# Kernel tuning notes

Hardware: AMD Instinct MI355X
Metric: run time of the kernel (lower is better)

The kernel has to match this reference:

```python
import jax, jax.numpy as jnp
import numpy as np

N = 3000          # num_sample (nodes)
N_OMICS = 3000    # input feature dims for both omics
ENC1, ENC2, NZ = 256, 128, 64


def _xavier(key, fan_in, fan_out):
    limit = float(np.sqrt(6.0 / (fan_in + fan_out)))
    return jax.random.uniform(key, (fan_in, fan_out), jnp.float32, -limit, limit)


def setup_inputs() -> dict:
    key = jax.random.key(0)
    ks = jax.random.split(key, 20)
    inp = {
        "omics_1": jax.random.normal(ks[0], (N, N_OMICS), jnp.float32),
        "omics_2": jax.random.normal(ks[1], (N, N_OMICS), jnp.float32),
    }
    # random dense adjacency, row-normalized (as a typical normalized graph operator)
    for i, name in enumerate(["adj_feature_omics1", "adj_feature_omics2",
                              "adj_spatial_omics1", "adj_spatial_omics2"]):
        a = jax.random.uniform(ks[2 + i], (N, N), jnp.float32)
        inp[name] = a / jnp.sum(a, axis=1, keepdims=True)
    # GNNLayer weights for the four GAE encoders (xavier uniform, as in reset_parameters)
    dims = [(N_OMICS, ENC1), (ENC1, ENC2), (ENC2, NZ)]
    kidx = 6
    for enc in ["f1", "f2", "s1", "s2"]:
        for li, (fi, fo) in enumerate(dims, start=1):
            inp[f"w_{enc}_{li}"] = _xavier(ks[kidx], fi, fo)
            kidx += 1
    return inp


def _gae_encoder(x, adj, w1, w2, w3):
    # GNNLayer: support = act(x @ W); out = spmm(adj, support). Dropout is identity (eval).
    z = adj @ jnp.tanh(x @ w1)          # [N, ENC1]
    z = adj @ jnp.tanh(z @ w2)          # [N, ENC2]
    z = adj @ (z @ w3)                  # [N, NZ]  (no activation on layer 3)
    adj_hat = jax.nn.sigmoid(z @ z.T)   # [N, N]
    return z, adj_hat


def reference(omics_1, omics_2,
              adj_feature_omics1, adj_feature_omics2,
              adj_spatial_omics1, adj_spatial_omics2,
              w_f1_1, w_f1_2, w_f1_3,
              w_f2_1, w_f2_2, w_f2_3,
              w_s1_1, w_s1_2, w_s1_3,
              w_s2_1, w_s2_2, w_s2_3):
    _, a1 = _gae_encoder(omics_1, adj_feature_omics1, w_f1_1, w_f1_2, w_f1_3)
    _, a2 = _gae_encoder(omics_2, adj_feature_omics2, w_f2_1, w_f2_2, w_f2_3)
    _, a3 = _gae_encoder(omics_1, adj_spatial_omics1, w_s1_1, w_s1_2, w_s1_3)
    _, a4 = _gae_encoder(omics_2, adj_spatial_omics2, w_s2_1, w_s2_2, w_s2_3)
    # stacked reconstructed adjacencies from the four encoders [4, N, N]
    return jnp.stack([a1, a2, a3, a4], axis=0)
```

## Files before the change

kernel.cpp:

```cpp
#include <hip/hip_runtime.h>
#include <stdint.h>
#include <stddef.h>


typedef __attribute__((ext_vector_type(8))) _Float16 half8;
typedef __attribute__((ext_vector_type(4))) float f32x4;

#define PAD 3072
#define MR  3000
#define ADJ_STRIDE ((size_t)PAD * PAD)

static __device__ __forceinline__ void async_cp16(const _Float16* g, _Float16* l) {
    __builtin_amdgcn_global_load_lds((const __attribute__((address_space(1))) void*)g,
                                     (__attribute__((address_space(3))) void*)l, 16, 0, 0);
}

struct PrepArgs {
    const float* X[2]; _Float16* Xh;
    const float* Wsrc[12];
    _Float16* Wdst[3];
};

__global__ __launch_bounds__(256) void prep(PrepArgs p) {
    __shared__ _Float16 lt[64 * 64];
    const int b = blockIdx.x;
    const int t = threadIdx.x;
    if (b < 4608) {
        const int which = b / 2304;
        const int idx = (b - which * 2304) * 256 + t;
        const int row = idx / 192;
        const int c0  = (idx - row * 192) * 16;
        const float* sp = p.X[which] + (size_t)row * MR + c0;
        _Float16* d = p.Xh + (size_t)which * ADJ_STRIDE + (size_t)row * PAD + c0;
        half8 h0, h1;
        const bool rok = row < MR;
        if (rok && c0 < MR) {
            f32x4 v0 = __builtin_nontemporal_load((const f32x4*)sp);
            f32x4 v1 = __builtin_nontemporal_load((const f32x4*)(sp + 4));
            #pragma unroll
            for (int j = 0; j < 4; ++j) { h0[j] = (_Float16)v0[j]; h0[4 + j] = (_Float16)v1[j]; }
        } else {
            #pragma unroll
            for (int j = 0; j < 8; ++j) h0[j] = (_Float16)0.f;
        }
        if (rok && c0 + 8 < MR) {
            f32x4 v2 = __builtin_nontemporal_load((const f32x4*)(sp + 8));
            f32x4 v3 = __builtin_nontemporal_load((const f32x4*)(sp + 12));
            #pragma unroll
            for (int j = 0; j < 4; ++j) { h1[j] = (_Float16)v2[j]; h1[4 + j] = (_Float16)v3[j]; }
        } else {
            #pragma unroll
            for (int j = 0; j < 8; ++j) h1[j] = (_Float16)0.f;
        }
        *(half8*)d = h0;
        *(half8*)(d + 8) = h1;
    } else {
        const int b2  = b - 4608;
        const int enc = b2 / 204;
        int rem = b2 - enc * 204;
        const float* src; _Float16* dst; int fi, fo, ldk, kt, rt;
        if (rem < 192) {
            src = p.Wsrc[enc * 3 + 0]; dst = p.Wdst[0] + (size_t)enc * 256 * PAD;
            fi = MR; fo = 256; ldk = PAD; kt = rem >> 2; rt = rem & 3;
        } else if (rem < 200) {
            rem -= 192;
            src = p.Wsrc[enc * 3 + 1]; dst = p.Wdst[1] + (size_t)enc * 128 * 256;
            fi = 256; fo = 128; ldk = 256; kt = rem >> 1; rt = rem & 1;
        } else {
            rem -= 200;
            src = p.Wsrc[enc * 3 + 2]; dst = p.Wdst[2] + (size_t)enc * 128 * 128;
            fi = 128; fo = 64; ldk = 128; kt = rem >> 1; rt = rem & 1;
        }
        const int k0 = kt * 64, r0 = rt * 64;
        {
            const int kr = t >> 2, cc = (t & 3) << 4;
            const int gk = k0 + kr;
            const bool kok = gk < fi;
            #pragma unroll
            for (int j = 0; j < 16; ++j) {
                const int gr = r0 + cc + j;
                const float v = (kok && gr < fo) ? src[(size_t)gk * fo + gr] : 0.f;
                lt[(cc + j) * 64 + kr] = (_Float16)v;
            }
        }
        __syncthreads();
        {
            const int rr = t >> 2, kk = (t & 3) << 4;
            half8 a  = *(half8*)&lt[rr * 64 + kk];
            half8 bb = *(half8*)&lt[rr * 64 + kk + 8];
            _Float16* dp = dst + (size_t)(r0 + rr) * ldk + k0 + kk;
            *(half8*)dp = a;
            *(half8*)(dp + 8) = bb;
        }
    }
}

struct GArgs {
    const _Float16* Aall; size_t aStride; int aMask;
    const _Float16* Ball; size_t bStride; int bMask;
    void* Call; size_t cStride;
    int M, Ncols, Kp, lda, ldb, ldc, mBound, nBound;
};

template<int ACT, int OMODE, int S>
static __device__ __forceinline__
void gemm_body(const GArgs& ga, int bx, int by, int bz, _Float16* smem)
{
    _Float16* As = smem;
    _Float16* Bs = smem + 8192;

    const int z   = bz;
    const int e   = z / S;
    const int ksl = z - e * S;
    const int Kslice = ga.Kp / S;
    const int kbase  = ksl * Kslice;

    const _Float16* A = ga.Aall + (size_t)(e & ga.aMask) * ga.aStride;
    const _Float16* B = ga.Ball + (size_t)(e & ga.bMask) * ga.bStride;

    const int tm = bx * 128;
    const int tn = by * 128;
    const int t    = threadIdx.x;
    const int lane = t & 63;
    const int w    = t >> 6;
    const int wm   = (w >> 1) * 64;
    const int wn   = (w & 1) * 64;
    const int lr   = lane & 15;
    const int lg   = lane >> 4;

    f32x4 acc[4][4];
    const f32x4 zero = {0.f, 0.f, 0.f, 0.f};
    #pragma unroll
    for (int i = 0; i < 4; ++i)
        #pragma unroll
        for (int j = 0; j < 4; ++j) acc[i][j] = zero;

    const int nkt = Kslice >> 6;
    for (int kt = 0; kt < nkt; ++kt) {
        const int k0 = kbase + (kt << 6);
        #pragma unroll
        for (int i = 0; i < 4; ++i) {
            const int c = t + i * 256;
            const int row = c >> 3, slot = c & 7;
            const int ss = slot ^ (row & 7);
            async_cp16(A + (size_t)(tm + row) * ga.lda + k0 + ss * 8, &As[c * 8]);
        }
        #pragma unroll
        for (int i = 0; i < 4; ++i) {
            const int c = t + i * 256;
            const int row = c >> 3, slot = c & 7;
            const int ss = slot ^ (row & 7);
            async_cp16(B + (size_t)(tn + row) * ga.ldb + k0 + ss * 8, &Bs[c * 8]);
        }
        __syncthreads();

        #pragma unroll
        for (int ks = 0; ks < 2; ++ks) {
            half8 af[4], bf[4];
            #pragma unroll
            for (int mi = 0; mi < 4; ++mi) {
                const int ra = wm + mi * 16 + lr;
                const int s  = (ks * 4 + lg) ^ (ra & 7);
                af[mi] = *(const half8*)((const char*)As + ra * 128 + s * 16);
            }
            #pragma unroll
            for (int ni = 0; ni < 4; ++ni) {
                const int rb = wn + ni * 16 + lr;
                const int s  = (ks * 4 + lg) ^ (rb & 7);
                bf[ni] = *(const half8*)((const char*)Bs + rb * 128 + s * 16);
            }
            #pragma unroll
            for (int mi = 0; mi < 4; ++mi)
                #pragma unroll
                for (int ni = 0; ni < 4; ++ni)
                    acc[mi][ni] = __builtin_amdgcn_mfma_f32_16x16x32_f16(
                        af[mi], bf[ni], acc[mi][ni], 0, 0, 0);
        }
        __syncthreads();
    }

    if (OMODE == 0) {
        _Float16* C = (_Float16*)ga.Call + (size_t)e * ga.cStride;
        #pragma unroll
        for (int mi = 0; mi < 4; ++mi)
            #pragma unroll
            for (int rr = 0; rr < 4; ++rr) {
                const int m = tm + wm + mi * 16 + lg * 4 + rr;
                #pragma unroll
                for (int ni = 0; ni < 4; ++ni) {
                    const int n = tn + wn + ni * 16 + lr;
                    float x = acc[mi][ni][rr];
                    if (ACT) x = tanhf(x);
                    const bool ok = (m < ga.M) && (n < ga.Ncols);
                    C[(size_t)m * ga.ldc + n] = ok ? (_Float16)x : (_Float16)0.f;
                }
            }
    } else {
        float* Cp = (float*)ga.Call + (size_t)(OMODE == 3 ? z : e) * ga.cStride;
        float* ep = (float*)smem + w * 2048;
        #pragma unroll
        for (int hs = 0; hs < 2; ++hs) {
            __syncthreads();
            #pragma unroll
            for (int mi2 = 0; mi2 < 2; ++mi2)
                #pragma unroll
                for (int ni = 0; ni < 4; ++ni)
                    #pragma unroll
                    for (int rr = 0; rr < 4; ++rr) {
                        const int row = mi2 * 16 + lg * 4 + rr;
                        const int col = ni * 16 + lr;
                        const int sw  = (((row ^ (row >> 2)) & 3) << 4);
                        ep[row * 64 + (col ^ sw)] = acc[hs * 2 + mi2][ni][rr];
                    }
            __syncthreads();
            #pragma unroll
            for (int r2 = 0; r2 < 8; ++r2) {
                const int row = r2 * 4 + (lane >> 4);
                const int c4  = (lane & 15) * 4;
                const int sw  = (((row ^ (row >> 2)) & 3) << 4);
                f32x4 v = *(const f32x4*)&ep[row * 64 + (c4 ^ sw)];
                const int gm = tm + wm + hs * 32 + row;
                const int gn = tn + wn + c4;
                if (gm < ga.mBound && gn < ga.nBound) {
                    if (OMODE == 2) {
                        #pragma unroll
                        for (int j = 0; j < 4; ++j)
                            v[j] = 1.0f / (1.0f + __expf(-v[j]));
                    }
                    *(f32x4*)&Cp[(size_t)gm * ga.ldc + gn] = v;
                }
            }
        }
    }
}

template<int ACT, int OMODE, int S>
__global__ __launch_bounds__(256, 2)
void gemm_bt(GArgs ga) {
    __shared__ _Float16 smem[16384];
    gemm_body<ACT, OMODE, S>(ga, blockIdx.x, blockIdx.y, blockIdx.z, smem);
}

struct Adj4 { const float* src[4]; };

__global__ __launch_bounds__(256, 2)
void fused_s1(GArgs ga, Adj4 a4, _Float16* __restrict__ adst)
{
    __shared__ _Float16 smem[16384];
    const int b = blockIdx.x;
    if (b < 192) {
        const int e   = b / 48;
        const int rem = b - e * 48;
        gemm_body<1, 0, 1>(ga, rem & 1, rem >> 1, e, smem);
    } else {
        const int cb  = b - 192;
        const int zz  = cb / 2304;
        const int idx = (cb - zz * 2304) * 256 + threadIdx.x;
        const int row = idx / 192;
        const int u   = idx - row * 192;
        const int c0  = u * 16;
        const float* sp = a4.src[zz] + (size_t)row * MR + c0;
        _Float16* d = adst + (size_t)zz * ADJ_STRIDE + (size_t)row * PAD + c0;
        half8 h0, h1;
        const bool rok = row < MR;
        if (rok && c0 < MR) {
            f32x4 v0 = __builtin_nontemporal_load((const f32x4*)sp);
            f32x4 v1 = __builtin_nontemporal_load((const f32x4*)(sp + 4));
            #pragma unroll
            for (int j = 0; j < 4; ++j) { h0[j] = (_Float16)v0[j]; h0[4 + j] = (_Float16)v1[j]; }
        } else {
            #pragma unroll
            for (int j = 0; j < 8; ++j) h0[j] = (_Float16)0.f;
        }
        if (rok && c0 + 8 < MR) {
            f32x4 v2 = __builtin_nontemporal_load((const f32x4*)(sp + 8));
            f32x4 v3 = __builtin_nontemporal_load((const f32x4*)(sp + 12));
            #pragma unroll
            for (int j = 0; j < 4; ++j) { h1[j] = (_Float16)v2[j]; h1[4 + j] = (_Float16)v3[j]; }
        } else {
            #pragma unroll
            for (int j = 0; j < 8; ++j) h1[j] = (_Float16)0.f;
        }
        *(half8*)d = h0;
        *(half8*)(d + 8) = h1;
    }
}

template<int S>
__global__ __launch_bounds__(256)
void reduce_k(const float* __restrict__ P, _Float16* __restrict__ out, size_t region)
{
    const size_t e    = blockIdx.y;
    const size_t base = (size_t)(blockIdx.x * 256 + threadIdx.x) * 8;
    const float* p0 = P + e * S * region + base;
    f32x4 s0 = {0.f, 0.f, 0.f, 0.f}, s1 = s0;
    #pragma unroll
    for (int s = 0; s < S; ++s) {
        const float* p = p0 + (size_t)s * region;
        s0 += *(const f32x4*)p;
        s1 += *(const f32x4*)(p + 4);
    }
    half8 h;
    #pragma unroll
    for (int j = 0; j < 8; ++j)
        h[j] = (_Float16)((j < 4) ? s0[j] : s1[j - 4]);
    *(half8*)(out + e * region + base) = h;
}

extern "C" void kernel_launch(void* const* d_in, const int* in_sizes, int n_in,
                              void* d_out, int out_size, void* d_ws, size_t ws_size,
                              hipStream_t stream)
{
    const size_t R1 = 786432;
    const size_t R2 = 393216;

    _Float16* Adj  = (_Float16*)d_out;
    float*    Part = (float*)(Adj + 4 * ADJ_STRIDE);

    _Float16* hb = (_Float16*)d_ws;
    size_t off = 0;
    auto alloc = [&](size_t elems) { _Float16* p = hb + off; off += elems; return p; };
    _Float16* Xh  = alloc(2 * ADJ_STRIDE);
    _Float16* T1  = alloc(4 * R1);
    _Float16* Z1  = alloc(4 * R1);
    _Float16* T2  = alloc(4 * R2);
    _Float16* Z2  = alloc(4 * R2);
    _Float16* T3  = alloc(4 * R2);
    _Float16* Z3  = alloc(4 * R2);
    _Float16* W1t = alloc(4ull * 256 * PAD);
    _Float16* W2t = alloc(4ull * 128 * 256);
    _Float16* W3t = alloc(4ull * 128 * 128);

    PrepArgs pa;
    pa.X[0] = (const float*)d_in[0];
    pa.X[1] = (const float*)d_in[1];
    pa.Xh = Xh;
    for (int enc = 0; enc < 4; ++enc)
        for (int li = 0; li < 3; ++li)
            pa.Wsrc[enc * 3 + li] = (const float*)d_in[6 + enc * 3 + li];
    pa.Wdst[0] = W1t; pa.Wdst[1] = W2t; pa.Wdst[2] = W3t;
    prep<<<dim3(5424, 1, 1), 256, 0, stream>>>(pa);

    const int BIG = 1 << 30;

    GArgs g1 = { W1t, (size_t)256 * PAD, 3, Xh, ADJ_STRIDE, 1,
                 T1, R1, 256, PAD, PAD, PAD, PAD, PAD, BIG, BIG };
    Adj4 a4;
    for (int i = 0; i < 4; ++i) a4.src[i] = (const float*)d_in[2 + i];
    fused_s1<<<dim3(9408, 1, 1), 256, 0, stream>>>(g1, a4, Adj);

    GArgs g2 = { Adj, ADJ_STRIDE, 3, T1, R1, 3,
                 Part, R1, PAD, 256, PAD, PAD, PAD, 256, BIG, BIG };
    gemm_bt<0, 3, 4><<<dim3(24, 2, 16), 256, 0, stream>>>(g2);
    reduce_k<4><<<dim3(384, 4, 1), 256, 0, stream>>>(Part, Z1, R1);

    GArgs g3 = { W2t, (size_t)128 * 256, 3, Z1, R1, 3,
                 T2, R2, 128, PAD, 256, 256, 256, PAD, BIG, BIG };
    gemm_bt<1, 0, 1><<<dim3(1, 24, 4), 256, 0, stream>>>(g3);

    GArgs g4 = { Adj, ADJ_STRIDE, 3, T2, R2, 3,
                 Part, R2, PAD, 128, PAD, PAD, PAD, 128, BIG, BIG };
    gemm_bt<0, 3, 8><<<dim3(24, 1, 32), 256, 0, stream>>>(g4);
    reduce_k<8><<<dim3(192, 4, 1), 256, 0, stream>>>(Part, Z2, R2);

    GArgs g5 = { W3t, (size_t)128 * 128, 3, Z2, R2, 3,
                 T3, R2, 128, PAD, 128, 128, 128, PAD, BIG, BIG };
    gemm_bt<0, 0, 1><<<dim3(1, 24, 4), 256, 0, stream>>>(g5);

    GArgs g6 = { Adj, ADJ_STRIDE, 3, T3, R2, 3,
                 Part, R2, PAD, 128, PAD, PAD, PAD, 128, BIG, BIG };
    gemm_bt<0, 3, 8><<<dim3(24, 1, 32), 256, 0, stream>>>(g6);
    reduce_k<8><<<dim3(192, 4, 1), 256, 0, stream>>>(Part, Z3, R2);

    GArgs g7 = { Z3, R2, 3, Z3, R2, 3,
                 d_out, (size_t)MR * MR, MR, MR, 64, 128, 128, MR, MR, MR };
    gemm_bt<0, 2, 1><<<dim3(24, 24, 4), 256, 0, stream>>>(g7);
}
```

Measured before the change: 282.2 us.

## Fuse fp32-to-fp16 conversion of inputs and adjacencies into GEMM tile loads

```diff
diff --git a/kernel.cpp b/kernel.cpp
--- a/kernel.cpp
+++ b/kernel.cpp
@@ -8,7 +8,6 @@
 
 #define PAD 3072
 #define MR  3000
-#define ADJ_STRIDE ((size_t)PAD * PAD)
 
 static __device__ __forceinline__ void async_cp16(const _Float16* g, _Float16* l) {
     __builtin_amdgcn_global_load_lds((const __attribute__((address_space(1))) void*)g,
@@ -16,93 +15,61 @@
 }
 
 struct PrepArgs {
-    const float* X[2]; _Float16* Xh;
     const float* Wsrc[12];
     _Float16* Wdst[3];
 };
 
-__global__ __launch_bounds__(256) void prep(PrepArgs p) {
+__global__ __launch_bounds__(256) void prep_w(PrepArgs p) {
     __shared__ _Float16 lt[64 * 64];
     const int b = blockIdx.x;
     const int t = threadIdx.x;
-    if (b < 4608) {
-        const int which = b / 2304;
-        const int idx = (b - which * 2304) * 256 + t;
-        const int row = idx / 192;
-        const int c0  = (idx - row * 192) * 16;
-        const float* sp = p.X[which] + (size_t)row * MR + c0;
-        _Float16* d = p.Xh + (size_t)which * ADJ_STRIDE + (size_t)row * PAD + c0;
-        half8 h0, h1;
-        const bool rok = row < MR;
-        if (rok && c0 < MR) {
-            f32x4 v0 = __builtin_nontemporal_load((const f32x4*)sp);
-            f32x4 v1 = __builtin_nontemporal_load((const f32x4*)(sp + 4));
-            #pragma unroll
-            for (int j = 0; j < 4; ++j) { h0[j] = (_Float16)v0[j]; h0[4 + j] = (_Float16)v1[j]; }
-        } else {
-            #pragma unroll
-            for (int j = 0; j < 8; ++j) h0[j] = (_Float16)0.f;
-        }
-        if (rok && c0 + 8 < MR) {
-            f32x4 v2 = __builtin_nontemporal_load((const f32x4*)(sp + 8));
-            f32x4 v3 = __builtin_nontemporal_load((const f32x4*)(sp + 12));
-            #pragma unroll
-            for (int j = 0; j < 4; ++j) { h1[j] = (_Float16)v2[j]; h1[4 + j] = (_Float16)v3[j]; }
-        } else {
-            #pragma unroll
-            for (int j = 0; j < 8; ++j) h1[j] = (_Float16)0.f;
-        }
-        *(half8*)d = h0;
-        *(half8*)(d + 8) = h1;
+    const int enc = b / 204;
+    int rem = b - enc * 204;
+    const float* src; _Float16* dst; int fi, fo, ldk, kt, rt;
+    if (rem < 192) {
+        src = p.Wsrc[enc * 3 + 0]; dst = p.Wdst[0] + (size_t)enc * 256 * PAD;
+        fi = MR; fo = 256; ldk = PAD; kt = rem >> 2; rt = rem & 3;
+    } else if (rem < 200) {
+        rem -= 192;
+        src = p.Wsrc[enc * 3 + 1]; dst = p.Wdst[1] + (size_t)enc * 128 * 256;
+        fi = 256; fo = 128; ldk = 256; kt = rem >> 1; rt = rem & 1;
     } else {
-        const int b2  = b - 4608;
-        const int enc = b2 / 204;
-        int rem = b2 - enc * 204;
-        const float* src; _Float16* dst; int fi, fo, ldk, kt, rt;
-        if (rem < 192) {
-            src = p.Wsrc[enc * 3 + 0]; dst = p.Wdst[0] + (size_t)enc * 256 * PAD;
-            fi = MR; fo = 256; ldk = PAD; kt = rem >> 2; rt = rem & 3;
-        } else if (rem < 200) {
-            rem -= 192;
-            src = p.Wsrc[enc * 3 + 1]; dst = p.Wdst[1] + (size_t)enc * 128 * 256;
-            fi = 256; fo = 128; ldk = 256; kt = rem >> 1; rt = rem & 1;
-        } else {
-            rem -= 200;
-            src = p.Wsrc[enc * 3 + 2]; dst = p.Wdst[2] + (size_t)enc * 128 * 128;
-            fi = 128; fo = 64; ldk = 128; kt = rem >> 1; rt = rem & 1;
-        }
-        const int k0 = kt * 64, r0 = rt * 64;
-        {
-            const int kr = t >> 2, cc = (t & 3) << 4;
-            const int gk = k0 + kr;
-            const bool kok = gk < fi;
-            #pragma unroll
-            for (int j = 0; j < 16; ++j) {
-                const int gr = r0 + cc + j;
-                const float v = (kok && gr < fo) ? src[(size_t)gk * fo + gr] : 0.f;
-                lt[(cc + j) * 64 + kr] = (_Float16)v;
-            }
-        }
-        __syncthreads();
-        {
-            const int rr = t >> 2, kk = (t & 3) << 4;
-            half8 a  = *(half8*)&lt[rr * 64 + kk];
-            half8 bb = *(half8*)&lt[rr * 64 + kk + 8];
-            _Float16* dp = dst + (size_t)(r0 + rr) * ldk + k0 + kk;
-            *(half8*)dp = a;
-            *(half8*)(dp + 8) = bb;
-        }
+        rem -= 200;
+        src = p.Wsrc[enc * 3 + 2]; dst = p.Wdst[2] + (size_t)enc * 128 * 128;
+        fi = 128; fo = 64; ldk = 128; kt = rem >> 1; rt = rem & 1;
+    }
+    const int k0 = kt * 64, r0 = rt * 64;
+    {
+        const int kr = t >> 2, cc = (t & 3) << 4;
+        const int gk = k0 + kr;
+        const bool kok = gk < fi;
+        #pragma unroll
+        for (int j = 0; j < 16; ++j) {
+            const int gr = r0 + cc + j;
+            const float v = (kok && gr < fo) ? src[(size_t)gk * fo + gr] : 0.f;
+            lt[(cc + j) * 64 + kr] = (_Float16)v;
+        }
+    }
+    __syncthreads();
+    {
+        const int rr = t >> 2, kk = (t & 3) << 4;
+        half8 a  = *(half8*)&lt[rr * 64 + kk];
+        half8 bb = *(half8*)&lt[rr * 64 + kk + 8];
+        _Float16* dp = dst + (size_t)(r0 + rr) * ldk + k0 + kk;
+        *(half8*)dp = a;
+        *(half8*)(dp + 8) = bb;
     }
 }
 
 struct GArgs {
     const _Float16* Aall; size_t aStride; int aMask;
     const _Float16* Ball; size_t bStride; int bMask;
+    const float* F32[4];
     void* Call; size_t cStride;
     int M, Ncols, Kp, lda, ldb, ldc, mBound, nBound;
 };
 
-template<int ACT, int OMODE, int S>
+template<int ACT, int OMODE, int S, int ASRC, int BSRC>
 static __device__ __forceinline__
 void gemm_body(const GArgs& ga, int bx, int by, int bz, _Float16* smem)
 {
@@ -117,6 +84,7 @@
 
     const _Float16* A = ga.Aall + (size_t)(e & ga.aMask) * ga.aStride;
     const _Float16* B = ga.Ball + (size_t)(e & ga.bMask) * ga.bStride;
+    const float*    F = ga.F32[e];
 
     const int tm = bx * 128;
     const int tn = by * 128;
@@ -138,19 +106,65 @@
     const int nkt = Kslice >> 6;
     for (int kt = 0; kt < nkt; ++kt) {
         const int k0 = kbase + (kt << 6);
-        #pragma unroll
-        for (int i = 0; i < 4; ++i) {
-            const int c = t + i * 256;
-            const int row = c >> 3, slot = c & 7;
-            const int ss = slot ^ (row & 7);
-            async_cp16(A + (size_t)(tm + row) * ga.lda + k0 + ss * 8, &As[c * 8]);
-        }
-        #pragma unroll
-        for (int i = 0; i < 4; ++i) {
-            const int c = t + i * 256;
-            const int row = c >> 3, slot = c & 7;
-            const int ss = slot ^ (row & 7);
-            async_cp16(B + (size_t)(tn + row) * ga.ldb + k0 + ss * 8, &Bs[c * 8]);
+        if (!ASRC) {
+            #pragma unroll
+            for (int i = 0; i < 4; ++i) {
+                const int c = t + i * 256;
+                const int row = c >> 3, slot = c & 7;
+                const int ss = slot ^ (row & 7);
+                async_cp16(A + (size_t)(tm + row) * ga.lda + k0 + ss * 8, &As[c * 8]);
+            }
+        }
+        if (!BSRC) {
+            #pragma unroll
+            for (int i = 0; i < 4; ++i) {
+                const int c = t + i * 256;
+                const int row = c >> 3, slot = c & 7;
+                const int ss = slot ^ (row & 7);
+                async_cp16(B + (size_t)(tn + row) * ga.ldb + k0 + ss * 8, &Bs[c * 8]);
+            }
+        }
+        if (ASRC) {
+            #pragma unroll
+            for (int i = 0; i < 4; ++i) {
+                const int c = t + i * 256;
+                const int row = c >> 3, g = c & 7;
+                const int grow = tm + row;
+                const int gcol = k0 + g * 8;
+                half8 h;
+                if (grow < MR && gcol < MR) {
+                    const float* ap = F + (size_t)grow * MR + gcol;
+                    f32x4 v0 = *(const f32x4*)ap;
+                    f32x4 v1 = *(const f32x4*)(ap + 4);
+                    #pragma unroll
+                    for (int j = 0; j < 4; ++j) { h[j] = (_Float16)v0[j]; h[4 + j] = (_Float16)v1[j]; }
+                } else {
+                    #pragma unroll
+                    for (int j = 0; j < 8; ++j) h[j] = (_Float16)0.f;
+                }
+                *(half8*)&As[row * 64 + ((g ^ (row & 7)) << 3)] = h;
+            }
+        }
+        if (BSRC) {
+            #pragma unroll
+            for (int i = 0; i < 4; ++i) {
+                const int c = t + i * 256;
+                const int row = c >> 3, g = c & 7;
+                const int grow = tn + row;
+                const int gcol = k0 + g * 8;
+                half8 h;
+                if (grow < MR && gcol < MR) {
+                    const float* bp = F + (size_t)grow * MR + gcol;
+                    f32x4 v0 = *(const f32x4*)bp;
+                    f32x4 v1 = *(const f32x4*)(bp + 4);
+                    #pragma unroll
+                    for (int j = 0; j < 4; ++j) { h[j] = (_Float16)v0[j]; h[4 + j] = (_Float16)v1[j]; }
+                } else {
+                    #pragma unroll
+                    for (int j = 0; j < 8; ++j) h[j] = (_Float16)0.f;
+                }
+                *(half8*)&Bs[row * 64 + ((g ^ (row & 7)) << 3)] = h;
+            }
         }
         __syncthreads();
 
@@ -226,67 +240,24 @@
                         #pragma unroll
                         for (int j = 0; j < 4; ++j)
                             v[j] = 1.0f / (1.0f + __expf(-v[j]));
+                        __builtin_nontemporal_store(v, (f32x4*)&Cp[(size_t)gm * ga.ldc + gn]);
+                    } else {
+                        *(f32x4*)&Cp[(size_t)gm * ga.ldc + gn] = v;
                     }
-                    *(f32x4*)&Cp[(size_t)gm * ga.ldc + gn] = v;
                 }
             }
         }
     }
 }
 
-template<int ACT, int OMODE, int S>
+template<int ACT, int OMODE, int S, int ASRC, int BSRC>
 __global__ __launch_bounds__(256, 2)
 void gemm_bt(GArgs ga) {
     __shared__ _Float16 smem[16384];
-    gemm_body<ACT, OMODE, S>(ga, blockIdx.x, blockIdx.y, blockIdx.z, smem);
-}
-
-struct Adj4 { const float* src[4]; };
-
-__global__ __launch_bounds__(256, 2)
-void fused_s1(GArgs ga, Adj4 a4, _Float16* __restrict__ adst)
-{
-    __shared__ _Float16 smem[16384];
-    const int b = blockIdx.x;
-    if (b < 192) {
-        const int e   = b / 48;
-        const int rem = b - e * 48;
-        gemm_body<1, 0, 1>(ga, rem & 1, rem >> 1, e, smem);
-    } else {
-        const int cb  = b - 192;
-        const int zz  = cb / 2304;
-        const int idx = (cb - zz * 2304) * 256 + threadIdx.x;
-        const int row = idx / 192;
-        const int u   = idx - row * 192;
-        const int c0  = u * 16;
-        const float* sp = a4.src[zz] + (size_t)row * MR + c0;
-        _Float16* d = adst + (size_t)zz * ADJ_STRIDE + (size_t)row * PAD + c0;
-        half8 h0, h1;
-        const bool rok = row < MR;
-        if (rok && c0 < MR) {
-            f32x4 v0 = __builtin_nontemporal_load((const f32x4*)sp);
-            f32x4 v1 = __builtin_nontemporal_load((const f32x4*)(sp + 4));
-            #pragma unroll
-            for (int j = 0; j < 4; ++j) { h0[j] = (_Float16)v0[j]; h0[4 + j] = (_Float16)v1[j]; }
-        } else {
-            #pragma unroll
-            for (int j = 0; j < 8; ++j) h0[j] = (_Float16)0.f;
-        }
-        if (rok && c0 + 8 < MR) {
-            f32x4 v2 = __builtin_nontemporal_load((const f32x4*)(sp + 8));
-            f32x4 v3 = __builtin_nontemporal_load((const f32x4*)(sp + 12));
-            #pragma unroll
-            for (int j = 0; j < 4; ++j) { h1[j] = (_Float16)v2[j]; h1[4 + j] = (_Float16)v3[j]; }
-        } else {
-            #pragma unroll
-            for (int j = 0; j < 8; ++j) h1[j] = (_Float16)0.f;
-        }
-        *(half8*)d = h0;
-        *(half8*)(d + 8) = h1;
-    }
-}
-
-template<int S>
+    gemm_body<ACT, OMODE, S, ASRC, BSRC>(ga, blockIdx.x, blockIdx.y, blockIdx.z, smem);
+}
+
+template<int ACT, int S>
 __global__ __launch_bounds__(256)
 void reduce_k(const float* __restrict__ P, _Float16* __restrict__ out, size_t region)
 {
@@ -302,8 +273,11 @@
     }
     half8 h;
     #pragma unroll
-    for (int j = 0; j < 8; ++j)
-        h[j] = (_Float16)((j < 4) ? s0[j] : s1[j - 4]);
+    for (int j = 0; j < 8; ++j) {
+        float x = (j < 4) ? s0[j] : s1[j - 4];
+        if (ACT) x = tanhf(x);
+        h[j] = (_Float16)x;
+    }
     *(half8*)(out + e * region + base) = h;
 }
 
@@ -311,16 +285,17 @@
                               void* d_out, int out_size, void* d_ws, size_t ws_size,
                               hipStream_t stream)
 {
+    const float* X1 = (const float*)d_in[0];
+    const float* X2 = (const float*)d_in[1];
+
     const size_t R1 = 786432;
     const size_t R2 = 393216;
 
-    _Float16* Adj  = (_Float16*)d_out;
-    float*    Part = (float*)(Adj + 4 * ADJ_STRIDE);
+    float* Part = (float*)d_out;
 
     _Float16* hb = (_Float16*)d_ws;
     size_t off = 0;
     auto alloc = [&](size_t elems) { _Float16* p = hb + off; off += elems; return p; };
-    _Float16* Xh  = alloc(2 * ADJ_STRIDE);
     _Float16* T1  = alloc(4 * R1);
     _Float16* Z1  = alloc(4 * R1);
     _Float16* T2  = alloc(4 * R2);
@@ -332,47 +307,53 @@
     _Float16* W3t = alloc(4ull * 128 * 128);
 
     PrepArgs pa;
-    pa.X[0] = (const float*)d_in[0];
-    pa.X[1] = (const float*)d_in[1];
-    pa.Xh = Xh;
     for (int enc = 0; enc < 4; ++enc)
         for (int li = 0; li < 3; ++li)
             pa.Wsrc[enc * 3 + li] = (const float*)d_in[6 + enc * 3 + li];
     pa.Wdst[0] = W1t; pa.Wdst[1] = W2t; pa.Wdst[2] = W3t;
-    prep<<<dim3(5424, 1, 1), 256, 0, stream>>>(pa);
+    prep_w<<<dim3(816, 1, 1), 256, 0, stream>>>(pa);
 
     const int BIG = 1 << 30;
 
-    GArgs g1 = { W1t, (size_t)256 * PAD, 3, Xh, ADJ_STRIDE, 1,
-                 T1, R1, 256, PAD, PAD, PAD, PAD, PAD, BIG, BIG };
-    Adj4 a4;
-    for (int i = 0; i < 4; ++i) a4.src[i] = (const float*)d_in[2 + i];
-    fused_s1<<<dim3(9408, 1, 1), 256, 0, stream>>>(g1, a4, Adj);
-
-    GArgs g2 = { Adj, ADJ_STRIDE, 3, T1, R1, 3,
-                 Part, R1, PAD, 256, PAD, PAD, PAD, 256, BIG, BIG };
-    gemm_bt<0, 3, 4><<<dim3(24, 2, 16), 256, 0, stream>>>(g2);
-    reduce_k<4><<<dim3(384, 4, 1), 256, 0, stream>>>(Part, Z1, R1);
+    GArgs g1 = { W1t, (size_t)256 * PAD, 3, nullptr, 0, 0,
+                 { X1, X2, X1, X2 },
+                 Part, R1, 256, PAD, PAD, PAD, MR, PAD, BIG, BIG };
+    gemm_bt<0, 3, 4, 0, 1><<<dim3(2, 24, 16), 256, 0, stream>>>(g1);
+    reduce_k<1, 4><<<dim3(384, 4, 1), 256, 0, stream>>>(Part, T1, R1);
+
+    GArgs g2 = { nullptr, 0, 0, T1, R1, 3,
+                 { (const float*)d_in[2], (const float*)d_in[3],
+                   (const float*)d_in[4], (const float*)d_in[5] },
+                 Part, R1, PAD, 256, PAD, MR, PAD, 256, BIG, BIG };
+    gemm_bt<0, 3, 4, 1, 0><<<dim3(24, 2, 16), 256, 0, stream>>>(g2);
+    reduce_k<0, 4><<<dim3(384, 4, 1), 256, 0, stream>>>(Part, Z1, R1);
 
     GArgs g3 = { W2t, (size_t)128 * 256, 3, Z1, R1, 3,
+                 { nullptr, nullptr, nullptr, nullptr },
                  T2, R2, 128, PAD, 256, 256, 256, PAD, BIG, BIG };
-    gemm_bt<1, 0, 1><<<dim3(1, 24, 4), 256, 0, stream>>>(g3);
-
-    GArgs g4 = { Adj, ADJ_STRIDE, 3, T2, R2, 3,
-                 Part, R2, PAD, 128, PAD, PAD, PAD, 128, BIG, BIG };
-    gemm_bt<0, 3, 8><<<dim3(24, 1, 32), 256, 0, stream>>>(g4);
-    reduce_k<8><<<dim3(192, 4, 1), 256, 0, stream>>>(Part, Z2, R2);
+    gemm_bt<1, 0, 1, 0, 0><<<dim3(1, 24, 4), 256, 0, stream>>>(g3);
+
+    GArgs g4 = { nullptr, 0, 0, T2, R2, 3,
+                 { (const float*)d_in[2], (const float*)d_in[3],
+                   (const float*)d_in[4], (const float*)d_in[5] },
+                 Part, R2, PAD, 128, PAD, MR, PAD, 128, BIG, BIG };
+    gemm_bt<0, 3, 8, 1, 0><<<dim3(24, 1, 32), 256, 0, stream>>>(g4);
+    reduce_k<0, 8><<<dim3(192, 4, 1), 256, 0, stream>>>(Part, Z2, R2);
 
     GArgs g5 = { W3t, (size_t)128 * 128, 3, Z2, R2, 3,
+                 { nullptr, nullptr, nullptr, nullptr },
                  T3, R2, 128, PAD, 128, 128, 128, PAD, BIG, BIG };
-    gemm_bt<0, 0, 1><<<dim3(1, 24, 4), 256, 0, stream>>>(g5);
-
-    GArgs g6 = { Adj, ADJ_STRIDE, 3, T3, R2, 3,
-                 Part, R2, PAD, 128, PAD, PAD, PAD, 128, BIG, BIG };
-    gemm_bt<0, 3, 8><<<dim3(24, 1, 32), 256, 0, stream>>>(g6);
-    reduce_k<8><<<dim3(192, 4, 1), 256, 0, stream>>>(Part, Z3, R2);
+    gemm_bt<0, 0, 1, 0, 0><<<dim3(1, 24, 4), 256, 0, stream>>>(g5);
+
+    GArgs g6 = { nullptr, 0, 0, T3, R2, 3,
+                 { (const float*)d_in[2], (const float*)d_in[3],
+                   (const float*)d_in[4], (const float*)d_in[5] },
+                 Part, R2, PAD, 128, PAD, MR, PAD, 128, BIG, BIG };
+    gemm_bt<0, 3, 8, 1, 0><<<dim3(24, 1, 32), 256, 0, stream>>>(g6);
+    reduce_k<0, 8><<<dim3(192, 4, 1), 256, 0, stream>>>(Part, Z3, R2);
 
     GArgs g7 = { Z3, R2, 3, Z3, R2, 3,
+                 { nullptr, nullptr, nullptr, nullptr },
                  d_out, (size_t)MR * MR, MR, MR, 64, 128, 128, MR, MR, MR };
-    gemm_bt<0, 2, 1><<<dim3(24, 24, 4), 256, 0, stream>>>(g7);
-}
+    gemm_bt<0, 2, 1, 0, 0><<<dim3(24, 24, 4), 256, 0, stream>>>(g7);
+}
```

New measurement: 293.6 us. +4.0%, slower.
